# Optimization experiments

Hardware: AMD Instinct MI355X
Metric: run time of the kernel (lower is better)

The kernel has to match this reference:

```python
import jax, jax.numpy as jnp
import numpy as np

N_HEADS = 12
N_GROUPS = 32
EPS = 1e-5


def setup_inputs() -> dict:
    key = jax.random.key(0)
    ks = jax.random.split(key, 6)
    B, C, H, W = 8, 768, 32, 32
    EC, S = 768, 256
    x = jax.random.normal(ks[0], (B, C, H, W), dtype=jnp.float32)
    encoder_out = jax.random.normal(ks[1], (B, EC, S), dtype=jnp.float32)
    gn_w = jnp.ones((C,), jnp.float32)
    gn_b = jnp.zeros((C,), jnp.float32)
    qkv_w = jax.random.normal(ks[2], (3 * C, C), dtype=jnp.float32) * 0.02
    qkv_b = jnp.zeros((3 * C,), jnp.float32)
    enc_w = jax.random.normal(ks[3], (2 * C, EC), dtype=jnp.float32) * 0.02
    enc_b = jnp.zeros((2 * C,), jnp.float32)
    proj_w = jax.random.normal(ks[4], (C, C), dtype=jnp.float32) * 0.02
    proj_b = jnp.zeros((C,), jnp.float32)
    return {"x": x, "encoder_out": encoder_out, "gn_w": gn_w, "gn_b": gn_b,
            "qkv_w": qkv_w, "qkv_b": qkv_b, "enc_w": enc_w, "enc_b": enc_b,
            "proj_w": proj_w, "proj_b": proj_b}


def _group_norm(x, w, b):
    # x: [B, C, T]
    B, C, T = x.shape
    xg = x.reshape(B, N_GROUPS, C // N_GROUPS, T)
    mean = jnp.mean(xg, axis=(2, 3), keepdims=True)
    var = jnp.var(xg, axis=(2, 3), keepdims=True)
    xn = ((xg - mean) * jax.lax.rsqrt(var + EPS)).reshape(B, C, T)
    return xn * w[None, :, None] + b[None, :, None]


def reference(x, encoder_out, gn_w, gn_b, qkv_w, qkv_b, enc_w, enc_b, proj_w, proj_b):
    B, C, Hs, Ws = x.shape
    T = Hs * Ws
    ch = C // N_HEADS
    xf = x.reshape(B, C, T)
    xn = _group_norm(xf, gn_w, gn_b)
    # 1x1 conv == channel matmul
    qkv = jnp.einsum('oc,bct->bot', qkv_w, xn) + qkv_b[None, :, None]  # [B, 3C, T]
    # torch layout: per-head contiguous blocks of [q, k, v]
    qkv = qkv.reshape(B * N_HEADS, 3 * ch, T)
    q, k, v = qkv[:, :ch], qkv[:, ch:2 * ch], qkv[:, 2 * ch:]
    ekv = jnp.einsum('oc,bcs->bos', enc_w, encoder_out) + enc_b[None, :, None]  # [B, 2C, S]
    ekv = ekv.reshape(B * N_HEADS, 2 * ch, -1)
    ek, ev = ekv[:, :ch], ekv[:, ch:]
    k = jnp.concatenate([ek, k], axis=-1)  # [BH, ch, S+T]
    v = jnp.concatenate([ev, v], axis=-1)
    scale = 1.0 / np.sqrt(np.sqrt(ch))
    w = jnp.einsum('bct,bcs->bts', q * scale, k * scale)  # [BH, T, S+T]
    w = jax.nn.softmax(w.astype(jnp.float32), axis=-1).astype(q.dtype)
    a = jnp.einsum('bts,bcs->bct', w, v).reshape(B, C, T)
    h = jnp.einsum('oc,bct->bot', proj_w, a) + proj_b[None, :, None]
    return (xf + h).reshape(B, C, Hs, Ws)
```

## Files before the change

kernel.cpp:

```cpp
#include <hip/hip_runtime.h>

typedef __attribute__((ext_vector_type(8))) short bf16x8;
typedef __attribute__((ext_vector_type(4))) float f32x4;
typedef __attribute__((ext_vector_type(16))) float f32x16;
typedef __attribute__((ext_vector_type(4))) float float4v;
typedef __attribute__((ext_vector_type(4))) unsigned short ushort4v;
typedef __attribute__((ext_vector_type(8))) unsigned short ushort8v;

#define DEVINL __device__ __forceinline__


DEVINL unsigned short f2bf(float f) {
  union { float f; unsigned u; } v; v.f = f;
  unsigned r = (v.u + 0x7fffu + ((v.u >> 16) & 1u)) >> 16;
  return (unsigned short)r;
}
DEVINL float bf2f(unsigned short h) {
  union { unsigned u; float f; } v; v.u = ((unsigned)h) << 16;
  return v.f;
}
DEVINL float exp2a(float x) {
  float r; asm("v_exp_f32 %0, %1" : "=v"(r) : "v"(x)); return r;
}
DEVINL unsigned cvtpk(float lo, float hi) {
  unsigned r;
  asm("v_cvt_pk_bf16_f32 %0, %1, %2" : "=v"(r) : "v"(lo), "v"(hi));
  return r;
}
DEVINL void gload16(const void* g, void* l) {
  __builtin_amdgcn_global_load_lds(
      (const __attribute__((address_space(1))) unsigned*)g,
      (__attribute__((address_space(3))) unsigned*)l, 16, 0, 0);
}
DEVINL void plswap(unsigned& a, unsigned& b) {
  asm("v_permlane32_swap_b32 %0, %1" : "+v"(a), "+v"(b));
}
DEVINL bf16x8 mkfrag(unsigned a, unsigned b, unsigned c, unsigned d) {
  union { unsigned u[4]; bf16x8 v; } x;
  x.u[0] = a; x.u[1] = b; x.u[2] = c; x.u[3] = d;
  return x.v;
}
#define WAITV4 asm volatile("s_waitcnt vmcnt(4)" ::: "memory")
#define WAITV0 asm volatile("s_waitcnt vmcnt(0)" ::: "memory")
#define RBAR  do { __builtin_amdgcn_s_barrier(); __builtin_amdgcn_sched_barrier(0); } while (0)

__global__ __launch_bounds__(256) void k_cvt3(const float* __restrict__ s0,
                                              const float* __restrict__ s1,
                                              const float* __restrict__ s2,
                                              unsigned short* __restrict__ d) {
  int i = blockIdx.x * 256 + threadIdx.x;
  const float* s; int off;
  if (i < 442368)      { s = s0; off = i; }
  else if (i < 737280) { s = s1; off = i - 442368; }
  else                 { s = s2; off = i - 737280; }
  float4v v = *(const float4v*)(s + (size_t)off * 4);
  ushort4v o;
  o[0] = f2bf(v[0]); o[1] = f2bf(v[1]); o[2] = f2bf(v[2]); o[3] = f2bf(v[3]);
  *(ushort4v*)(d + (size_t)i * 4) = o;
}

__global__ __launch_bounds__(256) void k_gn(const float* __restrict__ x,
                                            const float* __restrict__ gw,
                                            const float* __restrict__ gb,
                                            unsigned short* __restrict__ xnt) {
  int g = blockIdx.x, b = blockIdx.y, tid = threadIdx.x;
  const float* xb = x + ((size_t)b * 768 + g * 24) * 1024;
  float s = 0.f, ss = 0.f;
  for (int i = tid; i < 6144; i += 256) {
    float4v v = *(const float4v*)(xb + (size_t)i * 4);
    s += v[0] + v[1] + v[2] + v[3];
    ss += v[0] * v[0] + v[1] * v[1] + v[2] * v[2] + v[3] * v[3];
  }
  #pragma unroll
  for (int o = 32; o > 0; o >>= 1) { s += __shfl_down(s, o); ss += __shfl_down(ss, o); }
  __shared__ float rs[4], rss[4], stat[2];
  int w = tid >> 6;
  if ((tid & 63) == 0) { rs[w] = s; rss[w] = ss; }
  __syncthreads();
  if (tid == 0) {
    float S = rs[0] + rs[1] + rs[2] + rs[3], SS = rss[0] + rss[1] + rss[2] + rss[3];
    float mean = S / 24576.f;
    float var = SS / 24576.f - mean * mean;
    stat[0] = mean; stat[1] = rsqrtf(fmaxf(var, 0.f) + 1e-5f);
  }
  __syncthreads();
  float mean = stat[0], rstd = stat[1];
  float wv[24], bv[24];
  #pragma unroll
  for (int c = 0; c < 24; ++c) { wv[c] = gw[g * 24 + c]; bv[c] = gb[g * 24 + c]; }
  for (int it = 0; it < 4; ++it) {
    int t = it * 256 + tid;
    ushort8v ov[3];
    #pragma unroll
    for (int c = 0; c < 24; ++c) {
      float v = xb[(size_t)c * 1024 + t];
      ov[c >> 3][c & 7] = f2bf((v - mean) * rstd * wv[c] + bv[c]);
    }
    ushort8v* dst = (ushort8v*)(xnt + ((size_t)(b * 1024 + t)) * 768 + g * 24);
    dst[0] = ov[0]; dst[1] = ov[1]; dst[2] = ov[2];
  }
}

__global__ __launch_bounds__(256) void k_enc_tr(const float* __restrict__ enc,
                                                unsigned short* __restrict__ et) {
  int ct = blockIdx.x * 64, st = blockIdx.y * 64, b = blockIdx.z, tid = threadIdx.x;
  __shared__ unsigned short L[64 * 72];
  #pragma unroll
  for (int it = 0; it < 4; ++it) {
    int idx = it * 256 + tid; int r = idx >> 4, ch = idx & 15;
    float4v v = *(const float4v*)(enc + ((size_t)(b * 768 + ct + r)) * 256 + st + ch * 4);
    ushort4v o;
    o[0] = f2bf(v[0]); o[1] = f2bf(v[1]); o[2] = f2bf(v[2]); o[3] = f2bf(v[3]);
    *(ushort4v*)&L[r * 72 + ch * 4] = o;
  }
  __syncthreads();
  #pragma unroll
  for (int it = 0; it < 2; ++it) {
    int idx = it * 256 + tid; int s = idx >> 3, ch = idx & 7;
    ushort8v o;
    #pragma unroll
    for (int j = 0; j < 8; ++j) o[j] = L[(ch * 8 + j) * 72 + s];
    *(ushort8v*)(et + ((size_t)(b * 256 + st + s)) * 768 + ct + ch * 8) = o;
  }
}

__global__ __launch_bounds__(256) void k_vcat(const unsigned short* __restrict__ qkvt,
                                              const unsigned short* __restrict__ ekvt,
                                              unsigned short* __restrict__ vcat) {
  int s0 = blockIdx.x * 64, bh = blockIdx.y, b = bh / 12, h = bh % 12, tid = threadIdx.x;
  __shared__ unsigned short L[64 * 72];
  #pragma unroll
  for (int it = 0; it < 2; ++it) {
    int idx = it * 256 + tid; int s = idx >> 3, ch = idx & 7;
    int sg = s0 + s;
    const unsigned short* src = (sg < 256)
        ? ekvt + ((size_t)(b * 256 + sg)) * 1536 + h * 128 + 64 + ch * 8
        : qkvt + ((size_t)(b * 1024 + sg - 256)) * 2304 + h * 192 + 128 + ch * 8;
    *(ushort8v*)&L[s * 72 + ch * 8] = *(const ushort8v*)src;
  }
  __syncthreads();
  #pragma unroll
  for (int it = 0; it < 2; ++it) {
    int idx = it * 256 + tid; int c = idx >> 3, ch = idx & 7;
    ushort8v o;
    #pragma unroll
    for (int j = 0; j < 8; ++j) o[j] = L[(ch * 8 + j) * 72 + c];
    *(ushort8v*)(vcat + ((size_t)bh * 64 + c) * 1280 + s0 + ch * 8) = o;
  }
}

template <int EPI, int XGRP>
__global__ __launch_bounds__(256, 3) void k_gemm(const unsigned short* __restrict__ A,
                                                 const unsigned short* __restrict__ B,
                                                 const float* __restrict__ bias,
                                                 const float* __restrict__ resid,
                                                 void* __restrict__ outp,
                                                 int N, int K,
                                                 long sA, long sB, long sO, long sR) {
  int bz = blockIdx.z;
  int bx = blockIdx.x, by = blockIdx.y;
  if (XGRP > 0) {
    int L = blockIdx.x + gridDim.x * blockIdx.y;
    int g = L & 7, i = L >> 3;
    int ny = gridDim.y;
    bx = g * XGRP + i / ny;
    by = i % ny;
  }
  int m0 = bx * 128, n0 = by * 128;
  const unsigned short* Ab = A + (size_t)bz * sA + (size_t)m0 * K;
  const unsigned short* Bb = B + (size_t)bz * sB + (size_t)n0 * K;
  __shared__ unsigned short As[3][4096], Bs[3][4096];
  int tid = threadIdx.x, lane = tid & 63, w = tid >> 6;
  int ln = lane & 15, lg = lane >> 4;
  int wm = (w >> 1) * 64, wn = (w & 1) * 64;
  int sr = tid >> 2, sc = tid & 3;
  const unsigned short* gA = Ab + (size_t)sr * K + ((sc ^ (sr & 3)) * 8);
  const unsigned short* gB = Bb + (size_t)sr * K + ((sc ^ (sr & 3)) * 8);
  int swz = (lg ^ (ln & 3)) * 8;

  f32x4 acc[4][4];
  #pragma unroll
  for (int i = 0; i < 4; ++i)
    #pragma unroll
    for (int j = 0; j < 4; ++j) acc[i][j] = (f32x4){0.f, 0.f, 0.f, 0.f};

  auto stageAB = [&](int buf, int k0) {
    unsigned short* ad = &As[buf][0] + w * 512;
    unsigned short* bd = &Bs[buf][0] + w * 512;
    gload16(gA + k0, ad);
    gload16(gA + (size_t)64 * K + k0, ad + 2048);
    gload16(gB + k0, bd);
    gload16(gB + (size_t)64 * K + k0, bd + 2048);
  };
  auto comp = [&](int buf) {
    bf16x8 af[4], bfv[4];
    #pragma unroll
    for (int i = 0; i < 4; ++i) af[i] = *(const bf16x8*)&As[buf][(wm + i * 16 + ln) * 32 + swz];
    #pragma unroll
    for (int j = 0; j < 4; ++j) bfv[j] = *(const bf16x8*)&Bs[buf][(wn + j * 16 + ln) * 32 + swz];
    __builtin_amdgcn_s_setprio(1);
    #pragma unroll
    for (int i = 0; i < 4; ++i)
      #pragma unroll
      for (int j = 0; j < 4; ++j)
        acc[i][j] = __builtin_amdgcn_mfma_f32_16x16x32_bf16(af[i], bfv[j], acc[i][j], 0, 0, 0);
    __builtin_amdgcn_s_setprio(0);
  };

  int nk = K >> 5;
  stageAB(0, 0);
  stageAB(1, 32);
  WAITV4;
  RBAR;
  int cur = 0;
  for (int kt = 0; kt < nk - 2; ++kt) {
    int pre = cur - 1; if (pre < 0) pre += 3;
    stageAB(pre, (kt + 2) * 32);
    comp(cur);
    WAITV4;
    RBAR;
    ++cur; if (cur == 3) cur = 0;
  }
  comp(cur);
  WAITV0;
  RBAR;
  ++cur; if (cur == 3) cur = 0;
  comp(cur);

  #pragma unroll
  for (int i = 0; i < 4; ++i) {
    #pragma unroll
    for (int j = 0; j < 4; ++j) {
      #pragma unroll
      for (int r = 0; r < 4; ++r) {
        int row = m0 + wm + i * 16 + lg * 4 + r;
        int col = n0 + wn + j * 16 + ln;
        float v = acc[i][j][r];
        if (EPI == 0) {
          v += bias[col];
          ((unsigned short*)outp)[(size_t)bz * sO + (size_t)row * N + col] = f2bf(v);
        } else {
          v += bias[row] + resid[(size_t)bz * sR + (size_t)row * N + col];
          ((float*)outp)[(size_t)bz * sO + (size_t)row * N + col] = v;
        }
      }
    }
  }
}

__global__ __launch_bounds__(256, 3) void k_attn(const unsigned short* __restrict__ qkvt,
                                                 const unsigned short* __restrict__ ekvt,
                                                 const unsigned short* __restrict__ vcat,
                                                 unsigned short* __restrict__ at) {
  int bid = blockIdx.x;
  int swb = (bid & 7) * 96 + (bid >> 3);
  int t0 = (swb & 7) * 128, bh = swb >> 3, b = bh / 12, h = bh % 12;
  int tid = threadIdx.x, w = tid >> 6, lane = tid & 63;
  int ql = lane & 31, hi = lane >> 5;
  __shared__ unsigned short Ks[2][4096], Vs[2][4096];

  const float QSC = 0.125f * 1.44269504089f;
  bf16x8 aq[4];
  const unsigned short* qrow = qkvt + ((size_t)(b * 1024 + t0 + w * 32 + ql)) * 2304 + h * 192;
  #pragma unroll
  for (int jc = 0; jc < 4; ++jc) {
    ushort8v qv = *(const ushort8v*)(qrow + jc * 16 + hi * 8);
    bf16x8 o;
    #pragma unroll
    for (int e = 0; e < 8; ++e) o[e] = (short)f2bf(bf2f(qv[e]) * QSC);
    aq[jc] = o;
  }

  int rloc = w * 16 + (lane >> 3);
  int chunk = (lane & 7) ^ (lane >> 3);
  const unsigned short* ke_st = ekvt + ((size_t)(b * 256 + rloc)) * 1536 + h * 128 + chunk * 8;
  const unsigned short* kq_st = qkvt + ((long)b * 1024 - 256 + rloc) * 2304 + h * 192 + 64 + chunk * 8;
  const unsigned short* v_st  = vcat + ((size_t)(bh * 64 + rloc)) * 1280 + chunk * 8;
  unsigned short* kd = &Ks[0][0] + w * 1024;
  unsigned short* vd = &Vs[0][0] + w * 1024;

  auto stage = [&](int nb, int tn) {
    const unsigned short* ks;
    size_t rstep;
    if (tn < 4) { ks = ke_st + (size_t)tn * 64 * 1536; rstep = 8 * 1536; }
    else        { ks = kq_st + (size_t)tn * 64 * 2304; rstep = 8 * 2304; }
    unsigned short* kdd = kd + nb * 4096;
    unsigned short* vdd = vd + nb * 4096;
    const unsigned short* vs = v_st + tn * 64;
    gload16(ks, kdd);
    gload16(ks + rstep, kdd + 512);
    gload16(vs, vdd);
    gload16(vs + 8 * 1280, vdd + 512);
  };

  stage(0, 0);
  WAITV0;
  __syncthreads();

  f32x16 acc0, acc1;
  #pragma unroll
  for (int r = 0; r < 16; ++r) { acc0[r] = 0.f; acc1[r] = 0.f; }
  float l = 0.f;
  int xp = (ql & 7) << 4;

  for (int t = 0; t < 20; ++t) {
    int cur = t & 1;
    if (t < 19) stage(cur ^ 1, t + 1);

    f32x16 sf0, sf1;
    #pragma unroll
    for (int r = 0; r < 16; ++r) { sf0[r] = 0.f; sf1[r] = 0.f; }
    const char* kbase = (const char*)&Ks[cur][0] + ql * 128;
    __builtin_amdgcn_s_setprio(1);
    #pragma unroll
    for (int jc = 0; jc < 4; ++jc) {
      int off = (jc * 32 + hi * 16) ^ xp;
      bf16x8 k0f = *(const bf16x8*)(kbase + off);
      bf16x8 k1f = *(const bf16x8*)(kbase + 4096 + off);
      sf0 = __builtin_amdgcn_mfma_f32_32x32x16_bf16(k0f, aq[jc], sf0, 0, 0, 0);
      sf1 = __builtin_amdgcn_mfma_f32_32x32x16_bf16(k1f, aq[jc], sf1, 0, 0, 0);
    }
    __builtin_amdgcn_s_setprio(0);

    float pe[32];
    #pragma unroll
    for (int i = 0; i < 16; ++i) pe[i] = exp2a(sf0[i]);
    #pragma unroll
    for (int i = 0; i < 16; ++i) pe[16 + i] = exp2a(sf1[i]);

    const char* vbase = (const char*)&Vs[cur][0] + ql * 128;
    #pragma unroll
    for (int sb = 0; sb < 2; ++sb) {
      unsigned pk[8];
      #pragma unroll
      for (int i = 0; i < 8; ++i)
        pk[i] = cvtpk(pe[sb * 16 + 2 * i], pe[sb * 16 + 2 * i + 1]);
      plswap(pk[0], pk[2]);
      plswap(pk[1], pk[3]);
      plswap(pk[4], pk[6]);
      plswap(pk[5], pk[7]);
      bf16x8 fj0 = mkfrag(pk[0], pk[1], pk[2], pk[3]);
      bf16x8 fj1 = mkfrag(pk[4], pk[5], pk[6], pk[7]);
      __builtin_amdgcn_s_setprio(1);
      #pragma unroll
      for (int jj = 0; jj < 2; ++jj) {
        int off = (sb * 64 + jj * 32 + hi * 16) ^ xp;
        bf16x8 v0f = *(const bf16x8*)(vbase + off);
        bf16x8 v1f = *(const bf16x8*)(vbase + 4096 + off);
        bf16x8 pf = jj ? fj1 : fj0;
        acc0 = __builtin_amdgcn_mfma_f32_32x32x16_bf16(v0f, pf, acc0, 0, 0, 0);
        acc1 = __builtin_amdgcn_mfma_f32_32x32x16_bf16(v1f, pf, acc1, 0, 0, 0);
      }
      __builtin_amdgcn_s_setprio(0);
    }

    float s0 = 0.f, s1 = 0.f, s2 = 0.f, s3 = 0.f;
    #pragma unroll
    for (int i = 0; i < 8; ++i) {
      s0 += pe[i]; s1 += pe[8 + i]; s2 += pe[16 + i]; s3 += pe[24 + i];
    }
    l += (s0 + s1) + (s2 + s3);

    if (t < 19) WAITV0;
    __syncthreads();
  }

  l += __shfl_xor(l, 32);
  float rl = 1.f / l;
  unsigned short* orow = at + ((size_t)(b * 1024 + t0 + w * 32 + ql)) * 768 + h * 64;
  #pragma unroll
  for (int cb = 0; cb < 2; ++cb) {
    #pragma unroll
    for (int g = 0; g < 4; ++g) {
      int c = cb * 32 + g * 8 + hi * 4;
      ushort4v o;
      #pragma unroll
      for (int i = 0; i < 4; ++i) {
        float v = (cb ? acc1[g * 4 + i] : acc0[g * 4 + i]) * rl;
        o[i] = f2bf(v);
      }
      *(ushort4v*)(orow + c) = o;
    }
  }
}

extern "C" void kernel_launch(void* const* d_in, const int* in_sizes, int n_in,
                              void* d_out, int out_size, void* d_ws, size_t ws_size,
                              hipStream_t stream) {
  const float* x      = (const float*)d_in[0];
  const float* enc    = (const float*)d_in[1];
  const float* gn_w   = (const float*)d_in[2];
  const float* gn_b   = (const float*)d_in[3];
  const float* qkv_w  = (const float*)d_in[4];
  const float* qkv_b  = (const float*)d_in[5];
  const float* enc_w  = (const float*)d_in[6];
  const float* enc_b  = (const float*)d_in[7];
  const float* proj_w = (const float*)d_in[8];
  const float* proj_b = (const float*)d_in[9];
  float* out = (float*)d_out;

  char* ws = (char*)d_ws;
  unsigned short* w_qkv = (unsigned short*)(ws + 0);
  unsigned short* w_enc = (unsigned short*)(ws + 3538944);
  unsigned short* w_prj = (unsigned short*)(ws + 5898240);
  unsigned short* xn_t  = (unsigned short*)(ws + 7077888);
  unsigned short* enc_t = (unsigned short*)(ws + 19660800);
  unsigned short* qkv_t = (unsigned short*)(ws + 22806528);
  unsigned short* ekv_t = (unsigned short*)(ws + 60555264);
  unsigned short* vcat  = (unsigned short*)(ws + 66846720);
  unsigned short* a_t   = xn_t;

  k_cvt3<<<3456, 256, 0, stream>>>(qkv_w, enc_w, proj_w, w_qkv);
  k_gn<<<dim3(32, 8), 256, 0, stream>>>(x, gn_w, gn_b, xn_t);
  k_enc_tr<<<dim3(12, 4, 8), 256, 0, stream>>>(enc, enc_t);
  k_gemm<0, 8><<<dim3(64, 18, 1), 256, 0, stream>>>(xn_t, w_qkv, qkv_b, nullptr, qkv_t,
                                                    2304, 768, 0L, 0L, 0L, 0L);
  k_gemm<0, 2><<<dim3(16, 12, 1), 256, 0, stream>>>(enc_t, w_enc, enc_b, nullptr, ekv_t,
                                                    1536, 768, 0L, 0L, 0L, 0L);
  k_vcat<<<dim3(20, 96), 256, 0, stream>>>(qkv_t, ekv_t, vcat);
  k_attn<<<dim3(768), 256, 0, stream>>>(qkv_t, ekv_t, vcat, a_t);
  k_gemm<1, 0><<<dim3(6, 8, 8), 256, 0, stream>>>(w_prj, a_t, proj_b, x, out,
                                                  1024, 768, 0L, 786432L, 786432L, 786432L);
}
```

Before: 173.0 us.

## Rework GEMM to two-stage pipeline with BM template and split attention QK accumulators

Replaces the triple-buffered GEMM loop with a double-buffered one that has barriers before and after each stage refill. Adds a BM template so the encoder and projection GEMMs use 64-row tiles and launch more blocks. Also drops the tile-grouping swizzle and MFMA priority hints and raises the occupancy hint. In attention, the QK MFMA chain is split into two independent accumulators that are summed at the end, to shorten the dependency chain. The trade-offs are less prefetch depth, extra barriers, and possibly worse L2 locality without the swizzle.

```diff
diff --git a/kernel.cpp b/kernel.cpp
--- a/kernel.cpp
+++ b/kernel.cpp
@@ -40,9 +40,8 @@
   x.u[0] = a; x.u[1] = b; x.u[2] = c; x.u[3] = d;
   return x.v;
 }
-#define WAITV4 asm volatile("s_waitcnt vmcnt(4)" ::: "memory")
 #define WAITV0 asm volatile("s_waitcnt vmcnt(0)" ::: "memory")
-#define RBAR  do { __builtin_amdgcn_s_barrier(); __builtin_amdgcn_sched_barrier(0); } while (0)
+#define RBAR  __builtin_amdgcn_s_barrier()
 
 __global__ __launch_bounds__(256) void k_cvt3(const float* __restrict__ s0,
                                               const float* __restrict__ s1,
@@ -149,38 +148,31 @@
   }
 }
 
-template <int EPI, int XGRP>
-__global__ __launch_bounds__(256, 3) void k_gemm(const unsigned short* __restrict__ A,
+template <int EPI, int BM>
+__global__ __launch_bounds__(256, 4) void k_gemm(const unsigned short* __restrict__ A,
                                                  const unsigned short* __restrict__ B,
                                                  const float* __restrict__ bias,
                                                  const float* __restrict__ resid,
                                                  void* __restrict__ outp,
                                                  int N, int K,
                                                  long sA, long sB, long sO, long sR) {
+  constexpr int MI = BM / 32;
   int bz = blockIdx.z;
-  int bx = blockIdx.x, by = blockIdx.y;
-  if (XGRP > 0) {
-    int L = blockIdx.x + gridDim.x * blockIdx.y;
-    int g = L & 7, i = L >> 3;
-    int ny = gridDim.y;
-    bx = g * XGRP + i / ny;
-    by = i % ny;
-  }
-  int m0 = bx * 128, n0 = by * 128;
+  int m0 = blockIdx.x * BM, n0 = blockIdx.y * 128;
   const unsigned short* Ab = A + (size_t)bz * sA + (size_t)m0 * K;
   const unsigned short* Bb = B + (size_t)bz * sB + (size_t)n0 * K;
-  __shared__ unsigned short As[3][4096], Bs[3][4096];
+  __shared__ unsigned short As[2][BM * 32], Bs[2][128 * 32];
   int tid = threadIdx.x, lane = tid & 63, w = tid >> 6;
   int ln = lane & 15, lg = lane >> 4;
-  int wm = (w >> 1) * 64, wn = (w & 1) * 64;
+  int wm = (w >> 1) * (BM / 2), wn = (w & 1) * 64;
   int sr = tid >> 2, sc = tid & 3;
   const unsigned short* gA = Ab + (size_t)sr * K + ((sc ^ (sr & 3)) * 8);
   const unsigned short* gB = Bb + (size_t)sr * K + ((sc ^ (sr & 3)) * 8);
   int swz = (lg ^ (ln & 3)) * 8;
 
-  f32x4 acc[4][4];
-  #pragma unroll
-  for (int i = 0; i < 4; ++i)
+  f32x4 acc[MI][4];
+  #pragma unroll
+  for (int i = 0; i < MI; ++i)
     #pragma unroll
     for (int j = 0; j < 4; ++j) acc[i][j] = (f32x4){0.f, 0.f, 0.f, 0.f};
 
@@ -188,47 +180,49 @@
     unsigned short* ad = &As[buf][0] + w * 512;
     unsigned short* bd = &Bs[buf][0] + w * 512;
     gload16(gA + k0, ad);
-    gload16(gA + (size_t)64 * K + k0, ad + 2048);
+    if constexpr (BM == 128) gload16(gA + (size_t)64 * K + k0, ad + 2048);
     gload16(gB + k0, bd);
     gload16(gB + (size_t)64 * K + k0, bd + 2048);
   };
+  auto WAITP = [&] {
+    if constexpr (BM == 128) asm volatile("s_waitcnt vmcnt(4)" ::: "memory");
+    else                     asm volatile("s_waitcnt vmcnt(3)" ::: "memory");
+  };
   auto comp = [&](int buf) {
-    bf16x8 af[4], bfv[4];
-    #pragma unroll
-    for (int i = 0; i < 4; ++i) af[i] = *(const bf16x8*)&As[buf][(wm + i * 16 + ln) * 32 + swz];
+    bf16x8 af[MI], bfv[4];
+    #pragma unroll
+    for (int i = 0; i < MI; ++i) af[i] = *(const bf16x8*)&As[buf][(wm + i * 16 + ln) * 32 + swz];
     #pragma unroll
     for (int j = 0; j < 4; ++j) bfv[j] = *(const bf16x8*)&Bs[buf][(wn + j * 16 + ln) * 32 + swz];
-    __builtin_amdgcn_s_setprio(1);
-    #pragma unroll
-    for (int i = 0; i < 4; ++i)
+    #pragma unroll
+    for (int i = 0; i < MI; ++i)
       #pragma unroll
       for (int j = 0; j < 4; ++j)
         acc[i][j] = __builtin_amdgcn_mfma_f32_16x16x32_bf16(af[i], bfv[j], acc[i][j], 0, 0, 0);
-    __builtin_amdgcn_s_setprio(0);
   };
 
   int nk = K >> 5;
   stageAB(0, 0);
   stageAB(1, 32);
-  WAITV4;
+  WAITP();
   RBAR;
   int cur = 0;
-  for (int kt = 0; kt < nk - 2; ++kt) {
-    int pre = cur - 1; if (pre < 0) pre += 3;
-    stageAB(pre, (kt + 2) * 32);
+  for (int kt = 0; kt < nk; ++kt) {
     comp(cur);
-    WAITV4;
-    RBAR;
-    ++cur; if (cur == 3) cur = 0;
-  }
-  comp(cur);
-  WAITV0;
-  RBAR;
-  ++cur; if (cur == 3) cur = 0;
-  comp(cur);
-
-  #pragma unroll
-  for (int i = 0; i < 4; ++i) {
+    if (kt + 2 < nk) {
+      RBAR;
+      stageAB(cur, (kt + 2) * 32);
+      WAITP();
+      RBAR;
+    } else if (kt + 1 < nk) {
+      WAITV0;
+      RBAR;
+    }
+    cur ^= 1;
+  }
+
+  #pragma unroll
+  for (int i = 0; i < MI; ++i) {
     #pragma unroll
     for (int j = 0; j < 4; ++j) {
       #pragma unroll
@@ -307,9 +301,9 @@
     int cur = t & 1;
     if (t < 19) stage(cur ^ 1, t + 1);
 
-    f32x16 sf0, sf1;
-    #pragma unroll
-    for (int r = 0; r < 16; ++r) { sf0[r] = 0.f; sf1[r] = 0.f; }
+    f32x16 sA0, sB0, sA1, sB1;
+    #pragma unroll
+    for (int r = 0; r < 16; ++r) { sA0[r] = 0.f; sB0[r] = 0.f; sA1[r] = 0.f; sB1[r] = 0.f; }
     const char* kbase = (const char*)&Ks[cur][0] + ql * 128;
     __builtin_amdgcn_s_setprio(1);
     #pragma unroll
@@ -317,10 +311,17 @@
       int off = (jc * 32 + hi * 16) ^ xp;
       bf16x8 k0f = *(const bf16x8*)(kbase + off);
       bf16x8 k1f = *(const bf16x8*)(kbase + 4096 + off);
-      sf0 = __builtin_amdgcn_mfma_f32_32x32x16_bf16(k0f, aq[jc], sf0, 0, 0, 0);
-      sf1 = __builtin_amdgcn_mfma_f32_32x32x16_bf16(k1f, aq[jc], sf1, 0, 0, 0);
+      if (jc & 1) {
+        sB0 = __builtin_amdgcn_mfma_f32_32x32x16_bf16(k0f, aq[jc], sB0, 0, 0, 0);
+        sB1 = __builtin_amdgcn_mfma_f32_32x32x16_bf16(k1f, aq[jc], sB1, 0, 0, 0);
+      } else {
+        sA0 = __builtin_amdgcn_mfma_f32_32x32x16_bf16(k0f, aq[jc], sA0, 0, 0, 0);
+        sA1 = __builtin_amdgcn_mfma_f32_32x32x16_bf16(k1f, aq[jc], sA1, 0, 0, 0);
+      }
     }
     __builtin_amdgcn_s_setprio(0);
+    f32x16 sf0 = sA0 + sB0;
+    f32x16 sf1 = sA1 + sB1;
 
     float pe[32];
     #pragma unroll
@@ -413,12 +414,12 @@
   k_cvt3<<<3456, 256, 0, stream>>>(qkv_w, enc_w, proj_w, w_qkv);
   k_gn<<<dim3(32, 8), 256, 0, stream>>>(x, gn_w, gn_b, xn_t);
   k_enc_tr<<<dim3(12, 4, 8), 256, 0, stream>>>(enc, enc_t);
-  k_gemm<0, 8><<<dim3(64, 18, 1), 256, 0, stream>>>(xn_t, w_qkv, qkv_b, nullptr, qkv_t,
-                                                    2304, 768, 0L, 0L, 0L, 0L);
-  k_gemm<0, 2><<<dim3(16, 12, 1), 256, 0, stream>>>(enc_t, w_enc, enc_b, nullptr, ekv_t,
-                                                    1536, 768, 0L, 0L, 0L, 0L);
+  k_gemm<0, 128><<<dim3(64, 18, 1), 256, 0, stream>>>(xn_t, w_qkv, qkv_b, nullptr, qkv_t,
+                                                      2304, 768, 0L, 0L, 0L, 0L);
+  k_gemm<0, 64><<<dim3(32, 12, 1), 256, 0, stream>>>(enc_t, w_enc, enc_b, nullptr, ekv_t,
+                                                     1536, 768, 0L, 0L, 0L, 0L);
   k_vcat<<<dim3(20, 96), 256, 0, stream>>>(qkv_t, ekv_t, vcat);
   k_attn<<<dim3(768), 256, 0, stream>>>(qkv_t, ekv_t, vcat, a_t);
-  k_gemm<1, 0><<<dim3(6, 8, 8), 256, 0, stream>>>(w_prj, a_t, proj_b, x, out,
-                                                  1024, 768, 0L, 786432L, 786432L, 786432L);
-}
+  k_gemm<1, 64><<<dim3(12, 8, 8), 256, 0, stream>>>(w_prj, a_t, proj_b, x, out,
+                                                    1024, 768, 0L, 786432L, 786432L, 786432L);
+}
```

Result: no change. 174.3 us (+0.7%).
